# Optimization experiments

Hardware: AMD Instinct MI355X
Metric: run time of the kernel (lower is better)

The kernel has to match this reference:

```python
import jax, jax.numpy as jnp
import numpy as np

NEG = -10000.0
START, STOP = 4, 5
NT = 6  # 4 emotions + START + STOP
B, T, V = 512, 2048, 100000


def setup_inputs():
    key = jax.random.key(0)
    ks = jax.random.split(key, 7)
    transitions = jax.random.normal(ks[0], (NT, NT), jnp.float32)
    transitions = transitions.at[START, :].set(NEG).at[:, STOP].set(NEG)
    weight_for_emo_shift = jax.random.normal(ks[1], (4,), jnp.float32)
    multiplier = jax.random.normal(ks[2], (4, 4), jnp.float32)
    multiplier = multiplier.at[jnp.arange(4), jnp.arange(4)].set(NEG)
    out_table = jax.random.normal(ks[3], (V, 4), jnp.float32)
    bias = jax.random.uniform(ks[4], (B, T), jnp.float32)
    sentence = jax.random.randint(ks[5], (B, T), 0, V)
    tags = jax.random.randint(ks[6], (B, T), 0, 4)
    return {"transitions": transitions, "weight_for_emo_shift": weight_for_emo_shift,
            "multiplier": multiplier, "out_table": out_table, "bias": bias,
            "sentence": sentence, "tags": tags}


def _feats(out_table, sentence):
    # sentence: [T] int -> feats [T, 6]; cols 0..3 from out_table lookup,
    # col 4 = +3 at first turn else -3, col 5 = +3 at last turn else -3.
    t = sentence.shape[0]
    emo = out_table[sentence]                                      # [T,4]
    col4 = jnp.full((t,), -3.0, out_table.dtype).at[0].set(3.0)
    col5 = jnp.full((t,), -3.0, out_table.dtype).at[t - 1].set(3.0)
    return jnp.concatenate([emo, col4[:, None], col5[:, None]], axis=1)


def _nll_one(transitions, w, M, feats, bias, tags):
    # CRF forward algorithm (log-partition) minus gold path score for one dialog.
    t = feats.shape[0]

    def step(alpha, inp):
        feat, b = inp                                              # feat [6], b scalar
        shift = b * jnp.tanh((b - 0.5) * w)                        # [4]
        te = transitions.at[:4, :4].add(M * shift[None, :])        # [next, prev]
        alpha = jax.nn.logsumexp(alpha[None, :] + te, axis=1) + feat
        return alpha, None

    alpha0 = jnp.full((NT,), NEG, feats.dtype).at[START].set(0.0)
    alphaT, _ = jax.lax.scan(step, alpha0, (feats, bias))
    fwd = jax.nn.logsumexp(alphaT + transitions[STOP])

    # gold score
    prev = jnp.concatenate([jnp.array([START], tags.dtype), tags[:-1]])
    pc = jnp.clip(prev, 0, 3)
    ar = jnp.arange(t)
    shift = bias[:, None] * jnp.tanh((bias[:, None] - 0.5) * w[None, :])  # [T,4]
    biased = shift[ar, pc] * M[tags, pc]
    use_bias = (tags < 4) & (prev < 4)
    trans_s = transitions[tags, prev] + jnp.where(use_bias, biased, 0.0)
    gold = jnp.sum(trans_s + feats[ar, tags]) + transitions[STOP, tags[-1]]
    return fwd - gold


def reference(transitions, weight_for_emo_shift, multiplier, out_table, bias, sentence, tags):
    # multiplier: softmax over dim 0, then diagonal forced to -1 (as in the
    # in-place .data mutations in the original loop).
    M = jax.nn.softmax(multiplier, axis=0)
    M = M.at[jnp.arange(4), jnp.arange(4)].set(-1.0)
    feats = jax.vmap(lambda s: _feats(out_table, s))(sentence)     # [B,T,6]
    nll = jax.vmap(lambda f, b, tg: _nll_one(transitions, weight_for_emo_shift, M, f, b, tg))(feats, bias, tags)
    return nll                                                     # [B]
```

## Files before the change

kernel.cpp:

```cpp
#include <hip/hip_runtime.h>

#define TT 2048
#define BB 512

#if __has_builtin(__builtin_amdgcn_exp2f)
__device__ __forceinline__ float fexp2(float x){ return __builtin_amdgcn_exp2f(x); }
#else
__device__ __forceinline__ float fexp2(float x){ return exp2f(x); }
#endif
#if __has_builtin(__builtin_amdgcn_logf)
__device__ __forceinline__ float flog2(float x){ return __builtin_amdgcn_logf(x); }
#else
__device__ __forceinline__ float flog2(float x){ return log2f(x); }
#endif
__device__ __forceinline__ float frcp(float x){ return __builtin_amdgcn_rcpf(x); }

#if __has_builtin(__builtin_amdgcn_cvt_pk_fp8_f32) && __has_builtin(__builtin_amdgcn_cvt_pk_f32_fp8)
__device__ __forceinline__ unsigned enc_lo(float a,float b,unsigned old){
  return (unsigned)__builtin_amdgcn_cvt_pk_fp8_f32(a,b,(int)old,false);
}
__device__ __forceinline__ unsigned enc_hi(float a,float b,unsigned old){
  return (unsigned)__builtin_amdgcn_cvt_pk_fp8_f32(a,b,(int)old,true);
}
__device__ __forceinline__ void dec_lo(unsigned w,float&x,float&y){
  auto r=__builtin_amdgcn_cvt_pk_f32_fp8((int)w,false); x=r[0]; y=r[1];
}
__device__ __forceinline__ void dec_hi(unsigned w,float&x,float&y){
  auto r=__builtin_amdgcn_cvt_pk_f32_fp8((int)w,true); x=r[0]; y=r[1];
}
#else
__device__ __forceinline__ unsigned enc1(float x){
  if (!(x > 0x1p-10f)) return 0u;
  unsigned b = __float_as_uint(x) + 0x80000u;
  int e = (int)((b>>23)&0xFF) - 127;
  if (e < -6){ int m = (int)(x*512.0f + 0.5f); return (unsigned)m; }
  if (e > 8) return 0x7Eu;
  return (unsigned)(((e+7)<<3) | ((b>>20)&7));
}
__device__ __forceinline__ float dec1(unsigned byte){
  unsigned e=(byte>>3)&0xF, m=byte&7;
  if (e==0) return (float)m * 0x1p-9f;
  return __uint_as_float(((e+120u)<<23)|(m<<20));
}
__device__ __forceinline__ unsigned enc_lo(float a,float b,unsigned old){
  return (old & 0xFFFF0000u) | enc1(a) | (enc1(b)<<8);
}
__device__ __forceinline__ unsigned enc_hi(float a,float b,unsigned old){
  return (old & 0x0000FFFFu) | (enc1(a)<<16) | (enc1(b)<<24);
}
__device__ __forceinline__ void dec_lo(unsigned w,float&x,float&y){ x=dec1(w&0xFF); y=dec1((w>>8)&0xFF); }
__device__ __forceinline__ void dec_hi(unsigned w,float&x,float&y){ x=dec1((w>>16)&0xFF); y=dec1(w>>24); }
#endif

__device__ __forceinline__ float lse2_4(float x0,float x1,float x2,float x3){
  float m = fmaxf(fmaxf(x0,x1),fmaxf(x2,x3));
  float e = fexp2(x0-m)+fexp2(x1-m)+fexp2(x2-m)+fexp2(x3-m);
  return m + flog2(e);
}

__global__ __launch_bounds__(256) void crf_part(
    const float* __restrict__ trans,
    const float* __restrict__ w,
    const float* __restrict__ mult,
    const float* __restrict__ out_table,
    const float* __restrict__ bias,
    const int*   __restrict__ sentence,
    const int*   __restrict__ tags,
    float* __restrict__ partM,
    float* __restrict__ partG)
{
  constexpr float INVLN2 = 1.4426950408889634f;
  const int blk = blockIdx.x;
  const int b   = blk >> 2;
  const int p   = blk & 3;
  const int tid = threadIdx.x;

  __shared__ __align__(16) char  s_te[8192];
  __shared__ __align__(16) float s_c[512];
  __shared__ float s_PAm[64*16];
  __shared__ float s_PAs[64*4];
  __shared__ float s_M[16];
  __shared__ float s_tr[36];
  __shared__ float s_wgold[4];
  float* s_PBm = (float*)s_te;
  float* s_PBs = (float*)(s_te + 4096);

  float trans2[16]; float t2max = -1e30f;
  #pragma unroll
  for (int i=0;i<4;i++)
    #pragma unroll
    for (int k=0;k<4;k++){
      float v = trans[i*6+k]*INVLN2;
      trans2[i*4+k] = v; t2max = fmaxf(t2max, v);
    }
  const float T144 = t2max + 1.4427f;

  float M[16];
  {
    float e[16]; float cs[4]={0.f,0.f,0.f,0.f};
    #pragma unroll
    for (int i=0;i<4;i++)
      #pragma unroll
      for (int j=0;j<4;j++){
        float v = fexp2(mult[i*4+j]*INVLN2);
        e[i*4+j]=v; cs[j]+=v;
      }
    #pragma unroll
    for (int j=0;j<4;j++) cs[j]=frcp(cs[j]);
    #pragma unroll
    for (int i=0;i<4;i++)
      #pragma unroll
      for (int j=0;j<4;j++)
        M[i*4+j] = (i==j) ? -1.f : e[i*4+j]*cs[j];
  }
  const float wc0=w[0]*2.f*INVLN2, wc1=w[1]*2.f*INVLN2,
              wc2=w[2]*2.f*INVLN2, wc3=w[3]*2.f*INVLN2;
  if (tid<36) s_tr[tid]=trans[tid];
  if (tid==0){
    #pragma unroll
    for (int i=0;i<16;i++) s_M[i]=M[i];
  }
  __syncthreads();

  float gold = 0.f;
  {
    const int t0    = tid<<1;
    const int gbase = b*TT + (p<<9) + t0;
    float2 bb2 = *reinterpret_cast<const float2*>(bias + gbase);
    int2  sen2 = *reinterpret_cast<const int2*>(sentence + gbase);
    int2  tg2  = *reinterpret_cast<const int2*>(tags + gbase);
    float4 ftA = *reinterpret_cast<const float4*>(out_table + (size_t)sen2.x*4);
    float4 ftB = *reinterpret_cast<const float4*>(out_table + (size_t)sen2.y*4);

    int pv0;
    if ((tid & 63)==0) pv0 = (p==0 && t0==0) ? 4 : tags[gbase-1];
    else               pv0 = __shfl_up(tg2.y, 1);

    #pragma unroll
    for (int e=0;e<2;e++){
      const int tl = t0 + e;
      float bb   = e ? bb2.y : bb2.x;
      float4 f4e = e ? ftB   : ftA;
      int tg     = e ? tg2.y : tg2.x;
      int pv     = e ? tg2.x : pv0;

      float bh = bb-0.5f;
      float y0=fexp2(bh*wc0); float sh0=bb*(y0-1.f)*frcp(y0+1.f);
      float y1=fexp2(bh*wc1); float sh1=bb*(y1-1.f)*frcp(y1+1.f);
      float y2=fexp2(bh*wc2); float sh2v=bb*(y2-1.f)*frcp(y2+1.f);
      float y3=fexp2(bh*wc3); float sh3=bb*(y3-1.f)*frcp(y3+1.f);
      float s20=sh0*INVLN2, s21=sh1*INVLN2, s22=sh2v*INVLN2, s23=sh3*INVLN2;
      float f20=f4e.x*INVLN2, f21=f4e.y*INVLN2, f22=f4e.z*INVLN2, f23=f4e.w*INVLN2;

      float ct  = fmaxf(fmaxf(f20,f21),fmaxf(f22,f23)) + T144;
      float off = 8.0f - ct;
      float o0=f20+off, o1=f21+off, o2=f22+off, o3=f23+off;
      float a00=fexp2(fmaf(M[ 0],s20,trans2[ 0]+o0));
      float a01=fexp2(fmaf(M[ 1],s21,trans2[ 1]+o0));
      float a02=fexp2(fmaf(M[ 2],s22,trans2[ 2]+o0));
      float a03=fexp2(fmaf(M[ 3],s23,trans2[ 3]+o0));
      float a10=fexp2(fmaf(M[ 4],s20,trans2[ 4]+o1));
      float a11=fexp2(fmaf(M[ 5],s21,trans2[ 5]+o1));
      float a12=fexp2(fmaf(M[ 6],s22,trans2[ 6]+o1));
      float a13=fexp2(fmaf(M[ 7],s23,trans2[ 7]+o1));
      float a20=fexp2(fmaf(M[ 8],s20,trans2[ 8]+o2));
      float a21=fexp2(fmaf(M[ 9],s21,trans2[ 9]+o2));
      float a22=fexp2(fmaf(M[10],s22,trans2[10]+o2));
      float a23=fexp2(fmaf(M[11],s23,trans2[11]+o2));
      float a30=fexp2(fmaf(M[12],s20,trans2[12]+o3));
      float a31=fexp2(fmaf(M[13],s21,trans2[13]+o3));
      float a32=fexp2(fmaf(M[14],s22,trans2[14]+o3));
      float a33=fexp2(fmaf(M[15],s23,trans2[15]+o3));

      unsigned d0=enc_lo(a00,a01,0u); d0=enc_hi(a02,a03,d0);
      unsigned d1=enc_lo(a10,a11,0u); d1=enc_hi(a12,a13,d1);
      unsigned d2=enc_lo(a20,a21,0u); d2=enc_hi(a22,a23,d2);
      unsigned d3=enc_lo(a30,a31,0u); d3=enc_hi(a32,a33,d3);
      int g = (tl ^ ((tl>>3)&7)) << 4;
      *reinterpret_cast<uint4*>(s_te+g) = make_uint4(d0,d1,d2,d3);
      s_c[tl] = ct;

      float term;
      if (pv>=4){
        term = s_tr[tg*6+4];
      } else {
        float shp=(pv==0)?sh0:(pv==1)?sh1:(pv==2)?sh2v:sh3;
        term = s_tr[tg*6+pv] + shp*s_M[tg*4+pv];
      }
      term += (tg==0)?f4e.x:(tg==1)?f4e.y:(tg==2)?f4e.z:f4e.w;
      if (p==3 && tl==511) term += s_tr[30+tg];
      gold += term;
    }
    if (p==0 && tid==0){
      *reinterpret_cast<uint4*>(s_te) = make_uint4(0x38u,0x3800u,0x380000u,0x38000000u);
      s_c[0] = 8.0f;
    }
  }
  #pragma unroll
  for (int off=32; off>0; off>>=1) gold += __shfl_down(gold, off);
  if ((tid & 63)==0) s_wgold[tid>>6] = gold;
  __syncthreads();

  {
    int c = tid>>2, j = tid&3;
    int t0c = c<<3;
    int K = c & 7;
    float p0=(j==0)?1.f:0.f, p1=(j==1)?1.f:0.f, p2=(j==2)?1.f:0.f, p3=(j==3)?1.f:0.f;
    #pragma unroll
    for (int s=0;s<8;s++){
      int g = ((t0c+s) ^ K) << 4;
      uint4 q = *reinterpret_cast<const uint4*>(s_te + g);
      float e0,e1,e2,e3;
      dec_lo(q.x,e0,e1); dec_hi(q.x,e2,e3);
      float n0 = fmaf(e0,p0, e1*p1); n0 = fmaf(e2,p2,n0); n0 = fmaf(e3,p3,n0);
      dec_lo(q.y,e0,e1); dec_hi(q.y,e2,e3);
      float n1 = fmaf(e0,p0, e1*p1); n1 = fmaf(e2,p2,n1); n1 = fmaf(e3,p3,n1);
      dec_lo(q.z,e0,e1); dec_hi(q.z,e2,e3);
      float n2 = fmaf(e0,p0, e1*p1); n2 = fmaf(e2,p2,n2); n2 = fmaf(e3,p3,n2);
      dec_lo(q.w,e0,e1); dec_hi(q.w,e2,e3);
      float n3 = fmaf(e0,p0, e1*p1); n3 = fmaf(e2,p2,n3); n3 = fmaf(e3,p3,n3);
      p0=n0; p1=n1; p2=n2; p3=n3;
    }
    float sum = fmaxf((p0+p1)+(p2+p3), 1e-30f);
    float inv = frcp(sum);
    const float4* cp = reinterpret_cast<const float4*>(s_c + t0c);
    float4 ca=cp[0], cb=cp[1];
    float L = flog2(sum)
            + ((ca.x+ca.y)+(ca.z+ca.w)) + ((cb.x+cb.y)+(cb.z+cb.w)) - 64.0f;
    s_PAm[c*16 + 0*4 + j] = p0*inv;
    s_PAm[c*16 + 1*4 + j] = p1*inv;
    s_PAm[c*16 + 2*4 + j] = p2*inv;
    s_PAm[c*16 + 3*4 + j] = p3*inv;
    s_PAs[c*4 + j] = L;
  }
  __syncthreads();

  float *srcM = s_PAm, *srcS = s_PAs, *dstM = s_PBm, *dstS = s_PBs;
  #pragma unroll 1
  for (int n=32; n>=1; n>>=1){
    if (tid < n*4){
      int q = tid>>2, j = tid&3;
      const float* Am = srcM + (2*q)*16;
      const float* As = srcS + (2*q)*4;
      const float* Bm = Am + 16;
      const float* Bs = As + 4;
      float b0=Bs[0], b1=Bs[1], b2=Bs[2], b3=Bs[3];
      float m = fmaxf(fmaxf(b0,b1), fmaxf(b2,b3));
      float a0 = Am[0*4+j]*fexp2(b0-m);
      float a1 = Am[1*4+j]*fexp2(b1-m);
      float a2 = Am[2*4+j]*fexp2(b2-m);
      float a3 = Am[3*4+j]*fexp2(b3-m);
      float c0 = fmaf(Bm[ 0],a0, fmaf(Bm[ 1],a1, fmaf(Bm[ 2],a2, Bm[ 3]*a3)));
      float c1 = fmaf(Bm[ 4],a0, fmaf(Bm[ 5],a1, fmaf(Bm[ 6],a2, Bm[ 7]*a3)));
      float c2 = fmaf(Bm[ 8],a0, fmaf(Bm[ 9],a1, fmaf(Bm[10],a2, Bm[11]*a3)));
      float c3 = fmaf(Bm[12],a0, fmaf(Bm[13],a1, fmaf(Bm[14],a2, Bm[15]*a3)));
      float ssum = fmaxf((c0+c1)+(c2+c3), 1e-37f);
      float inv = frcp(ssum);
      dstM[q*16+0*4+j] = c0*inv;
      dstM[q*16+1*4+j] = c1*inv;
      dstM[q*16+2*4+j] = c2*inv;
      dstM[q*16+3*4+j] = c3*inv;
      dstS[q*4+j] = m + As[j] + flog2(ssum);
    }
    __syncthreads();
    float* tm;
    tm=srcM; srcM=dstM; dstM=tm;
    tm=srcS; srcS=dstS; dstS=tm;
  }

  const int idx = (b<<2) | p;
  if (tid < 16)      partM[idx*20 + tid] = srcM[tid];
  else if (tid < 20) partM[idx*20 + tid] = srcS[tid-16];
  if (tid == 32)
    partG[idx] = ((s_wgold[0]+s_wgold[1])+(s_wgold[2]+s_wgold[3]));
}

__global__ __launch_bounds__(256) void crf_final(
    const float* __restrict__ trans,
    const float* __restrict__ out_table,
    const int*   __restrict__ sentence,
    const float* __restrict__ partM,
    const float* __restrict__ partG,
    float* __restrict__ out)
{
  constexpr float INVLN2 = 1.4426950408889634f;
  constexpr float LN2    = 0.6931471805599453f;
  const int tid = threadIdx.x;
  const int j   = tid & 3;
  const int dd  = tid >> 2;
  const int d   = (blockIdx.x<<6) + dd;

  __shared__ float s_m[64][21];

  const float* P0 = partM + (size_t)(d<<2)*20;
  float c0=P0[0+j], c1=P0[4+j], c2=P0[8+j], c3=P0[12+j];
  float Lc=P0[16+j];
  #pragma unroll
  for (int q=1;q<4;q++){
    const float* Bq = partM + (size_t)((d<<2)+q)*20;
    float b0=Bq[16], b1=Bq[17], b2=Bq[18], b3=Bq[19];
    float m = fmaxf(fmaxf(b0,b1), fmaxf(b2,b3));
    float a0=c0*fexp2(b0-m), a1=c1*fexp2(b1-m),
          a2=c2*fexp2(b2-m), a3=c3*fexp2(b3-m);
    float n0 = fmaf(Bq[ 0],a0, fmaf(Bq[ 1],a1, fmaf(Bq[ 2],a2, Bq[ 3]*a3)));
    float n1 = fmaf(Bq[ 4],a0, fmaf(Bq[ 5],a1, fmaf(Bq[ 6],a2, Bq[ 7]*a3)));
    float n2 = fmaf(Bq[ 8],a0, fmaf(Bq[ 9],a1, fmaf(Bq[10],a2, Bq[11]*a3)));
    float n3 = fmaf(Bq[12],a0, fmaf(Bq[13],a1, fmaf(Bq[14],a2, Bq[15]*a3)));
    float ss = fmaxf((n0+n1)+(n2+n3), 1e-37f);
    float iv = frcp(ss);
    c0=n0*iv; c1=n1*iv; c2=n2*iv; c3=n3*iv;
    Lc += m + flog2(ss);
  }
  s_m[dd][0+j]=c0; s_m[dd][4+j]=c1; s_m[dd][8+j]=c2; s_m[dd][12+j]=c3;
  s_m[dd][16+j]=Lc;
  __syncthreads();

  if (j==0){
    const float* Pf = s_m[dd];
    const float* Ls = s_m[dd]+16;
    int s0 = sentence[(size_t)d*TT];
    float4 f0 = *reinterpret_cast<const float4*>(out_table + (size_t)s0*4);
    float a0 = (trans[ 4] + f0.x)*INVLN2;
    float a1 = (trans[10] + f0.y)*INVLN2;
    float a2 = (trans[16] + f0.z)*INVLN2;
    float a3 = (trans[22] + f0.w)*INVLN2;
    float u0 = Ls[0]+a0, u1 = Ls[1]+a1, u2 = Ls[2]+a2, u3 = Ls[3]+a3;
    float m2 = fmaxf(fmaxf(u0,u1), fmaxf(u2,u3));
    float e0 = fexp2(u0-m2), e1 = fexp2(u1-m2), e2 = fexp2(u2-m2), e3 = fexp2(u3-m2);
    float v0 = fmaf(Pf[ 0],e0, fmaf(Pf[ 1],e1, fmaf(Pf[ 2],e2, Pf[ 3]*e3)));
    float v1 = fmaf(Pf[ 4],e0, fmaf(Pf[ 5],e1, fmaf(Pf[ 6],e2, Pf[ 7]*e3)));
    float v2 = fmaf(Pf[ 8],e0, fmaf(Pf[ 9],e1, fmaf(Pf[10],e2, Pf[11]*e3)));
    float v3 = fmaf(Pf[12],e0, fmaf(Pf[13],e1, fmaf(Pf[14],e2, Pf[15]*e3)));
    float n0 = flog2(v0)+m2, n1 = flog2(v1)+m2, n2 = flog2(v2)+m2, n3 = flog2(v3)+m2;
    float fwd2 = lse2_4(n0+trans[30]*INVLN2, n1+trans[31]*INVLN2,
                        n2+trans[32]*INVLN2, n3+trans[33]*INVLN2);
    const float* Gp = partG + (size_t)(d<<2);
    float g = (Gp[0]+Gp[1])+(Gp[2]+Gp[3]);
    out[d] = fwd2*LN2 - g;
  }
}

extern "C" void kernel_launch(void* const* d_in, const int* in_sizes, int n_in,
                              void* d_out, int out_size, void* d_ws, size_t ws_size,
                              hipStream_t stream) {
  const float* trans     = (const float*)d_in[0];
  const float* w         = (const float*)d_in[1];
  const float* mult      = (const float*)d_in[2];
  const float* out_table = (const float*)d_in[3];
  const float* bias      = (const float*)d_in[4];
  const int*   sentence  = (const int*)d_in[5];
  const int*   tags      = (const int*)d_in[6];
  float* partM = (float*)d_ws;
  float* partG = (float*)((char*)d_ws + BB*4*20*sizeof(float));
  crf_part<<<BB*4, 256, 0, stream>>>(trans, w, mult, out_table, bias, sentence, tags,
                                     partM, partG);
  crf_final<<<BB/64, 256, 0, stream>>>(trans, out_table, sentence, partM, partG,
                                       (float*)d_out);
}
```

Measured before the change: 21.97 us.

## Drop block barriers in tree reduction, pack FP8 decode into vector FMA, compute M via lanes

The 32-to-1 tree reduction of chunk transfer matrices now runs its last five levels inside a single wavefront without __syncthreads, after one block-wide level. The per-step scale sums are reduced with shuffles instead of an s_c shared array. The FP8 transition tiles are stored transposed so the 8-step chain can use packed 2-wide FMAs. The softmax multiplier is computed across 16 lanes and broadcast with readlane. The aim is fewer block barriers and LDS round trips, but the barrier-free stage relies on lockstep wavefront execution and LDS ordering within a wave.

```diff
diff --git a/kernel.cpp b/kernel.cpp
--- a/kernel.cpp
+++ b/kernel.cpp
@@ -2,6 +2,15 @@
 
 #define TT 2048
 #define BB 512
+
+typedef float f2 __attribute__((ext_vector_type(2)));
+__device__ __forceinline__ f2 mk2(float v){ f2 r; r.x=v; r.y=v; return r; }
+
+#if __has_builtin(__builtin_elementwise_fma)
+#define FMA2(a,b,c) __builtin_elementwise_fma((a),(b),(c))
+#else
+#define FMA2(a,b,c) ((a)*(b)+(c))
+#endif
 
 #if __has_builtin(__builtin_amdgcn_exp2f)
 __device__ __forceinline__ float fexp2(float x){ return __builtin_amdgcn_exp2f(x); }
@@ -22,11 +31,11 @@
 __device__ __forceinline__ unsigned enc_hi(float a,float b,unsigned old){
   return (unsigned)__builtin_amdgcn_cvt_pk_fp8_f32(a,b,(int)old,true);
 }
-__device__ __forceinline__ void dec_lo(unsigned w,float&x,float&y){
-  auto r=__builtin_amdgcn_cvt_pk_f32_fp8((int)w,false); x=r[0]; y=r[1];
-}
-__device__ __forceinline__ void dec_hi(unsigned w,float&x,float&y){
-  auto r=__builtin_amdgcn_cvt_pk_f32_fp8((int)w,true); x=r[0]; y=r[1];
+__device__ __forceinline__ f2 dec_lo2(unsigned w){
+  auto r=__builtin_amdgcn_cvt_pk_f32_fp8((int)w,false); f2 o; o.x=r[0]; o.y=r[1]; return o;
+}
+__device__ __forceinline__ f2 dec_hi2(unsigned w){
+  auto r=__builtin_amdgcn_cvt_pk_f32_fp8((int)w,true); f2 o; o.x=r[0]; o.y=r[1]; return o;
 }
 #else
 __device__ __forceinline__ unsigned enc1(float x){
@@ -48,8 +57,8 @@
 __device__ __forceinline__ unsigned enc_hi(float a,float b,unsigned old){
   return (old & 0x0000FFFFu) | (enc1(a)<<16) | (enc1(b)<<24);
 }
-__device__ __forceinline__ void dec_lo(unsigned w,float&x,float&y){ x=dec1(w&0xFF); y=dec1((w>>8)&0xFF); }
-__device__ __forceinline__ void dec_hi(unsigned w,float&x,float&y){ x=dec1((w>>16)&0xFF); y=dec1(w>>24); }
+__device__ __forceinline__ f2 dec_lo2(unsigned w){ f2 o; o.x=dec1(w&0xFF); o.y=dec1((w>>8)&0xFF); return o; }
+__device__ __forceinline__ f2 dec_hi2(unsigned w){ f2 o; o.x=dec1((w>>16)&0xFF); o.y=dec1(w>>24); return o; }
 #endif
 
 __device__ __forceinline__ float lse2_4(float x0,float x1,float x2,float x3){
@@ -76,7 +85,6 @@
   const int tid = threadIdx.x;
 
   __shared__ __align__(16) char  s_te[8192];
-  __shared__ __align__(16) float s_c[512];
   __shared__ float s_PAm[64*16];
   __shared__ float s_PAs[64*4];
   __shared__ float s_M[16];
@@ -97,32 +105,24 @@
 
   float M[16];
   {
-    float e[16]; float cs[4]={0.f,0.f,0.f,0.f};
+    int l = tid & 15;
+    float mv = fexp2(mult[l]*INVLN2);
+    float s1 = mv + __shfl_xor(mv, 4);
+    float cs = s1 + __shfl_xor(s1, 8);
+    float Ml = ((l>>2)==(l&3)) ? -1.f : mv*frcp(cs);
+    if (tid < 16) s_M[tid] = Ml;
+    int mi = __float_as_int(Ml);
     #pragma unroll
-    for (int i=0;i<4;i++)
-      #pragma unroll
-      for (int j=0;j<4;j++){
-        float v = fexp2(mult[i*4+j]*INVLN2);
-        e[i*4+j]=v; cs[j]+=v;
-      }
-    #pragma unroll
-    for (int j=0;j<4;j++) cs[j]=frcp(cs[j]);
-    #pragma unroll
-    for (int i=0;i<4;i++)
-      #pragma unroll
-      for (int j=0;j<4;j++)
-        M[i*4+j] = (i==j) ? -1.f : e[i*4+j]*cs[j];
+    for (int i=0;i<16;i++)
+      M[i] = __int_as_float(__builtin_amdgcn_readlane(mi, i));
   }
   const float wc0=w[0]*2.f*INVLN2, wc1=w[1]*2.f*INVLN2,
               wc2=w[2]*2.f*INVLN2, wc3=w[3]*2.f*INVLN2;
   if (tid<36) s_tr[tid]=trans[tid];
-  if (tid==0){
-    #pragma unroll
-    for (int i=0;i<16;i++) s_M[i]=M[i];
-  }
   __syncthreads();
 
   float gold = 0.f;
+  float cts;
   {
     const int t0    = tid<<1;
     const int gbase = b*TT + (p<<9) + t0;
@@ -136,6 +136,7 @@
     if ((tid & 63)==0) pv0 = (p==0 && t0==0) ? 4 : tags[gbase-1];
     else               pv0 = __shfl_up(tg2.y, 1);
 
+    float ctv[2];
     #pragma unroll
     for (int e=0;e<2;e++){
       const int tl = t0 + e;
@@ -172,13 +173,13 @@
       float a32=fexp2(fmaf(M[14],s22,trans2[14]+o3));
       float a33=fexp2(fmaf(M[15],s23,trans2[15]+o3));
 
-      unsigned d0=enc_lo(a00,a01,0u); d0=enc_hi(a02,a03,d0);
-      unsigned d1=enc_lo(a10,a11,0u); d1=enc_hi(a12,a13,d1);
-      unsigned d2=enc_lo(a20,a21,0u); d2=enc_hi(a22,a23,d2);
-      unsigned d3=enc_lo(a30,a31,0u); d3=enc_hi(a32,a33,d3);
+      unsigned d0=enc_lo(a00,a10,0u); d0=enc_hi(a20,a30,d0);
+      unsigned d1=enc_lo(a01,a11,0u); d1=enc_hi(a21,a31,d1);
+      unsigned d2=enc_lo(a02,a12,0u); d2=enc_hi(a22,a32,d2);
+      unsigned d3=enc_lo(a03,a13,0u); d3=enc_hi(a23,a33,d3);
       int g = (tl ^ ((tl>>3)&7)) << 4;
       *reinterpret_cast<uint4*>(s_te+g) = make_uint4(d0,d1,d2,d3);
-      s_c[tl] = ct;
+      ctv[e] = ct;
 
       float term;
       if (pv>=4){
@@ -193,86 +194,114 @@
     }
     if (p==0 && tid==0){
       *reinterpret_cast<uint4*>(s_te) = make_uint4(0x38u,0x3800u,0x380000u,0x38000000u);
-      s_c[0] = 8.0f;
-    }
+      ctv[0] = 8.0f;
+    }
+    cts = ctv[0] + ctv[1];
   }
   #pragma unroll
   for (int off=32; off>0; off>>=1) gold += __shfl_down(gold, off);
   if ((tid & 63)==0) s_wgold[tid>>6] = gold;
+  float cpair = cts + __shfl_xor(cts, 1);
+  float csum  = cpair + __shfl_xor(cpair, 2);
   __syncthreads();
 
   {
     int c = tid>>2, j = tid&3;
     int t0c = c<<3;
     int K = c & 7;
-    float p0=(j==0)?1.f:0.f, p1=(j==1)?1.f:0.f, p2=(j==2)?1.f:0.f, p3=(j==3)?1.f:0.f;
+    f2 a01, a23;
+    a01.x = (j==0)?1.f:0.f; a01.y = (j==1)?1.f:0.f;
+    a23.x = (j==2)?1.f:0.f; a23.y = (j==3)?1.f:0.f;
     #pragma unroll
     for (int s=0;s<8;s++){
       int g = ((t0c+s) ^ K) << 4;
       uint4 q = *reinterpret_cast<const uint4*>(s_te + g);
-      float e0,e1,e2,e3;
-      dec_lo(q.x,e0,e1); dec_hi(q.x,e2,e3);
-      float n0 = fmaf(e0,p0, e1*p1); n0 = fmaf(e2,p2,n0); n0 = fmaf(e3,p3,n0);
-      dec_lo(q.y,e0,e1); dec_hi(q.y,e2,e3);
-      float n1 = fmaf(e0,p0, e1*p1); n1 = fmaf(e2,p2,n1); n1 = fmaf(e3,p3,n1);
-      dec_lo(q.z,e0,e1); dec_hi(q.z,e2,e3);
-      float n2 = fmaf(e0,p0, e1*p1); n2 = fmaf(e2,p2,n2); n2 = fmaf(e3,p3,n2);
-      dec_lo(q.w,e0,e1); dec_hi(q.w,e2,e3);
-      float n3 = fmaf(e0,p0, e1*p1); n3 = fmaf(e2,p2,n3); n3 = fmaf(e3,p3,n3);
-      p0=n0; p1=n1; p2=n2; p3=n3;
-    }
-    float sum = fmaxf((p0+p1)+(p2+p3), 1e-30f);
+      float p0=a01.x, p1=a01.y, p2=a23.x, p3=a23.y;
+      f2 n01 = dec_lo2(q.x)*mk2(p0);
+      f2 n23 = dec_hi2(q.x)*mk2(p0);
+      n01 = FMA2(dec_lo2(q.y), mk2(p1), n01);
+      n23 = FMA2(dec_hi2(q.y), mk2(p1), n23);
+      n01 = FMA2(dec_lo2(q.z), mk2(p2), n01);
+      n23 = FMA2(dec_hi2(q.z), mk2(p2), n23);
+      n01 = FMA2(dec_lo2(q.w), mk2(p3), n01);
+      n23 = FMA2(dec_hi2(q.w), mk2(p3), n23);
+      a01 = n01; a23 = n23;
+    }
+    float sum = fmaxf((a01.x+a01.y)+(a23.x+a23.y), 1e-30f);
     float inv = frcp(sum);
-    const float4* cp = reinterpret_cast<const float4*>(s_c + t0c);
-    float4 ca=cp[0], cb=cp[1];
-    float L = flog2(sum)
-            + ((ca.x+ca.y)+(ca.z+ca.w)) + ((cb.x+cb.y)+(cb.z+cb.w)) - 64.0f;
-    s_PAm[c*16 + 0*4 + j] = p0*inv;
-    s_PAm[c*16 + 1*4 + j] = p1*inv;
-    s_PAm[c*16 + 2*4 + j] = p2*inv;
-    s_PAm[c*16 + 3*4 + j] = p3*inv;
+    float L = flog2(sum) + csum - 64.0f;
+    s_PAm[c*16 + 0*4 + j] = a01.x*inv;
+    s_PAm[c*16 + 1*4 + j] = a01.y*inv;
+    s_PAm[c*16 + 2*4 + j] = a23.x*inv;
+    s_PAm[c*16 + 3*4 + j] = a23.y*inv;
     s_PAs[c*4 + j] = L;
   }
   __syncthreads();
 
-  float *srcM = s_PAm, *srcS = s_PAs, *dstM = s_PBm, *dstS = s_PBs;
-  #pragma unroll 1
-  for (int n=32; n>=1; n>>=1){
-    if (tid < n*4){
-      int q = tid>>2, j = tid&3;
-      const float* Am = srcM + (2*q)*16;
-      const float* As = srcS + (2*q)*4;
-      const float* Bm = Am + 16;
-      const float* Bs = As + 4;
-      float b0=Bs[0], b1=Bs[1], b2=Bs[2], b3=Bs[3];
-      float m = fmaxf(fmaxf(b0,b1), fmaxf(b2,b3));
-      float a0 = Am[0*4+j]*fexp2(b0-m);
-      float a1 = Am[1*4+j]*fexp2(b1-m);
-      float a2 = Am[2*4+j]*fexp2(b2-m);
-      float a3 = Am[3*4+j]*fexp2(b3-m);
-      float c0 = fmaf(Bm[ 0],a0, fmaf(Bm[ 1],a1, fmaf(Bm[ 2],a2, Bm[ 3]*a3)));
-      float c1 = fmaf(Bm[ 4],a0, fmaf(Bm[ 5],a1, fmaf(Bm[ 6],a2, Bm[ 7]*a3)));
-      float c2 = fmaf(Bm[ 8],a0, fmaf(Bm[ 9],a1, fmaf(Bm[10],a2, Bm[11]*a3)));
-      float c3 = fmaf(Bm[12],a0, fmaf(Bm[13],a1, fmaf(Bm[14],a2, Bm[15]*a3)));
-      float ssum = fmaxf((c0+c1)+(c2+c3), 1e-37f);
-      float inv = frcp(ssum);
-      dstM[q*16+0*4+j] = c0*inv;
-      dstM[q*16+1*4+j] = c1*inv;
-      dstM[q*16+2*4+j] = c2*inv;
-      dstM[q*16+3*4+j] = c3*inv;
-      dstS[q*4+j] = m + As[j] + flog2(ssum);
-    }
-    __syncthreads();
-    float* tm;
-    tm=srcM; srcM=dstM; dstM=tm;
-    tm=srcS; srcS=dstS; dstS=tm;
-  }
-
-  const int idx = (b<<2) | p;
-  if (tid < 16)      partM[idx*20 + tid] = srcM[tid];
-  else if (tid < 20) partM[idx*20 + tid] = srcS[tid-16];
-  if (tid == 32)
-    partG[idx] = ((s_wgold[0]+s_wgold[1])+(s_wgold[2]+s_wgold[3]));
+  if (tid < 128){
+    int q = tid>>2, j = tid&3;
+    const float* Am = s_PAm + (2*q)*16;
+    const float* As = s_PAs + (2*q)*4;
+    const float* Bm = Am + 16;
+    const float* Bs = As + 4;
+    float b0=Bs[0], b1=Bs[1], b2=Bs[2], b3=Bs[3];
+    float m = fmaxf(fmaxf(b0,b1), fmaxf(b2,b3));
+    float a0 = Am[0*4+j]*fexp2(b0-m);
+    float a1 = Am[1*4+j]*fexp2(b1-m);
+    float a2 = Am[2*4+j]*fexp2(b2-m);
+    float a3 = Am[3*4+j]*fexp2(b3-m);
+    float c0 = fmaf(Bm[ 0],a0, fmaf(Bm[ 1],a1, fmaf(Bm[ 2],a2, Bm[ 3]*a3)));
+    float c1 = fmaf(Bm[ 4],a0, fmaf(Bm[ 5],a1, fmaf(Bm[ 6],a2, Bm[ 7]*a3)));
+    float c2 = fmaf(Bm[ 8],a0, fmaf(Bm[ 9],a1, fmaf(Bm[10],a2, Bm[11]*a3)));
+    float c3 = fmaf(Bm[12],a0, fmaf(Bm[13],a1, fmaf(Bm[14],a2, Bm[15]*a3)));
+    float ssum = fmaxf((c0+c1)+(c2+c3), 1e-37f);
+    float inv = frcp(ssum);
+    s_PBm[q*16+0*4+j] = c0*inv;
+    s_PBm[q*16+1*4+j] = c1*inv;
+    s_PBm[q*16+2*4+j] = c2*inv;
+    s_PBm[q*16+3*4+j] = c3*inv;
+    s_PBs[q*4+j] = m + As[j] + flog2(ssum);
+  }
+  __syncthreads();
+
+  if (tid < 64){
+    float *srcM = s_PBm, *srcS = s_PBs, *dstM = s_PAm, *dstS = s_PAs;
+    #pragma unroll 1
+    for (int n=16; n>=1; n>>=1){
+      if (tid < n*4){
+        int q = tid>>2, j = tid&3;
+        const float* Am = srcM + (2*q)*16;
+        const float* As = srcS + (2*q)*4;
+        const float* Bm = Am + 16;
+        const float* Bs = As + 4;
+        float b0=Bs[0], b1=Bs[1], b2=Bs[2], b3=Bs[3];
+        float m = fmaxf(fmaxf(b0,b1), fmaxf(b2,b3));
+        float a0 = Am[0*4+j]*fexp2(b0-m);
+        float a1 = Am[1*4+j]*fexp2(b1-m);
+        float a2 = Am[2*4+j]*fexp2(b2-m);
+        float a3 = Am[3*4+j]*fexp2(b3-m);
+        float c0 = fmaf(Bm[ 0],a0, fmaf(Bm[ 1],a1, fmaf(Bm[ 2],a2, Bm[ 3]*a3)));
+        float c1 = fmaf(Bm[ 4],a0, fmaf(Bm[ 5],a1, fmaf(Bm[ 6],a2, Bm[ 7]*a3)));
+        float c2 = fmaf(Bm[ 8],a0, fmaf(Bm[ 9],a1, fmaf(Bm[10],a2, Bm[11]*a3)));
+        float c3 = fmaf(Bm[12],a0, fmaf(Bm[13],a1, fmaf(Bm[14],a2, Bm[15]*a3)));
+        float ssum = fmaxf((c0+c1)+(c2+c3), 1e-37f);
+        float inv = frcp(ssum);
+        dstM[q*16+0*4+j] = c0*inv;
+        dstM[q*16+1*4+j] = c1*inv;
+        dstM[q*16+2*4+j] = c2*inv;
+        dstM[q*16+3*4+j] = c3*inv;
+        dstS[q*4+j] = m + As[j] + flog2(ssum);
+      }
+      float* tm;
+      tm=srcM; srcM=dstM; dstM=tm;
+      tm=srcS; srcS=dstS; dstS=tm;
+    }
+    const int idx = (b<<2) | p;
+    if (tid < 16)      partM[idx*20 + tid] = srcM[tid];
+    else if (tid < 20) partM[idx*20 + tid] = srcS[tid-16];
+    if (tid == 20)
+      partG[idx] = ((s_wgold[0]+s_wgold[1])+(s_wgold[2]+s_wgold[3]));
+  }
 }
 
 __global__ __launch_bounds__(256) void crf_final(
```

Result: faster. 21.22 us (-3.4%).
